# Optimization experiments

Hardware: AMD Instinct MI355X
Metric: run time of the kernel (lower is better)

## Reference

```python
import jax, jax.numpy as jnp
import numpy as np

B = 32
N_IN = 65536
N_OUT = 65536
NNZ = 2097152  # ~32 connections per output unit


def setup_inputs() -> dict:
    key = jax.random.key(0)
    k_x, k_w, k_r, k_c = jax.random.split(key, 4)
    x = jax.random.normal(k_x, (B, N_IN), dtype=jnp.float32)
    # weight init mirrors torch: randn * (init_scale / sqrt(mean_fan_in))
    init_scale = 0.01
    fan_in_mean = float(NNZ) / float(N_OUT)
    weight = jax.random.normal(k_w, (NNZ,), dtype=jnp.float32) * (init_scale / np.sqrt(fan_in_mean))
    bias = jnp.zeros((N_OUT,), dtype=jnp.float32)
    # rows are sorted (concatenated per output j in the original __init__)
    rows = jnp.sort(jax.random.randint(k_r, (NNZ,), 0, N_OUT, dtype=jnp.int64))
    cols = jax.random.randint(k_c, (NNZ,), 0, N_IN, dtype=jnp.int64)
    return {"x": x, "weight": weight, "bias": bias, "rows": rows, "cols": cols, "N_out": N_OUT}


def reference(x, weight, bias, rows, cols, N_out):
    # gather input columns per connection, scale by per-edge weight: (B, nnz)
    weighted = x[:, cols] * weight[None, :]
    # batched scatter-add by output row: segment_sum over edges -> (N_out, B) -> (B, N_out)
    out = jax.ops.segment_sum(weighted.T, rows, num_segments=N_out,
                              indices_are_sorted=True).T
    return out + bias[None, :]
```

## Files before the change

kernel.cpp:

```cpp
#include <hip/hip_runtime.h>


typedef unsigned int u32;

static __device__ __forceinline__ u32 f2bf_bits(float f) {
  u32 b = __builtin_bit_cast(u32, f);
  return (b + 0x7fffu + ((b >> 16) & 1u)) >> 16;
}
static __device__ __forceinline__ float bf_lo(u32 u) {
  return __builtin_bit_cast(float, u << 16);
}
static __device__ __forceinline__ float bf_hi(u32 u) {
  return __builtin_bit_cast(float, u & 0xffff0000u);
}

__global__ __launch_bounds__(256) void prep_kernel(
    const float* __restrict__ x, u32* __restrict__ xTb,
    const int* __restrict__ rows, int* __restrict__ row_ptr,
    int n_in, int n_out, int nnz, int tblocks) {
  if ((int)blockIdx.x < tblocks) {
    __shared__ float t[32][65];
    int c0 = blockIdx.x * 64;
    if (c0 + 64 <= n_in) {
      const float4* x4 = (const float4*)x;
      for (int idx = threadIdx.x; idx < 32 * 16; idx += 256) {
        int b = idx >> 4, q = idx & 15;
        float4 v = x4[((size_t)b * n_in + c0) / 4 + q];
        t[b][q * 4 + 0] = v.x; t[b][q * 4 + 1] = v.y;
        t[b][q * 4 + 2] = v.z; t[b][q * 4 + 3] = v.w;
      }
    } else {
      for (int idx = threadIdx.x; idx < 32 * 64; idx += 256) {
        int b = idx >> 6, cl = idx & 63;
        int c = c0 + cl;
        t[b][cl] = (c < n_in) ? x[(size_t)b * n_in + c] : 0.f;
      }
    }
    __syncthreads();
    for (int idx = threadIdx.x; idx < 64 * 16; idx += 256) {
      int cl = idx >> 4, bp = idx & 15;
      int c = c0 + cl;
      if (c < n_in) {
        u32 v = f2bf_bits(t[2 * bp][cl]) | (f2bf_bits(t[2 * bp + 1][cl]) << 16);
        xTb[(size_t)c * 16 + bp] = v;
      }
    }
  } else {
    int e = ((int)blockIdx.x - tblocks) * 256 + threadIdx.x;
    if (e < nnz) {
      int r = rows[e];
      int rp = (e == 0) ? -1 : rows[e - 1];
      for (int j = rp + 1; j <= r; ++j) row_ptr[j] = e;
      if (e == nnz - 1)
        for (int j = r + 1; j <= n_out; ++j) row_ptr[j] = nnz;
    }
  }
}

__global__ __launch_bounds__(512, 8) void ll_main_bf16_kernel(
    const uint4* __restrict__ xTb4,
    const float* __restrict__ wgt,
    const float4* __restrict__ bias4,
    const int* __restrict__ cols,
    const int* __restrict__ row_ptr,
    float4* __restrict__ out4, int n_out) {
  __shared__ float tile[32][65];
  int tid = threadIdx.x;
  int lane = tid & 63;
  int l = lane & 3;
  int gw = lane >> 2;
  int wv = tid >> 6;
  int half = wv >> 2;
  int g = (wv & 3) * 16 + gw;
  int gb = lane & 60;
  int jb = blockIdx.x * 64;
  int j = jb + g;
  float a0 = 0, a1 = 0, a2 = 0, a3 = 0, a4 = 0, a5 = 0, a6 = 0, a7 = 0;
  if (j < n_out) {
    int s = row_ptr[j], e = row_ptr[j + 1];
    int last = e - 1;
    for (int base = s + half * 4; base < e; base += 8) {
      int il = min(base + l, last);
      int cl_ = cols[il];
      float wl_ = (base + l <= last) ? wgt[il] : 0.f;
#define EDGE_K(K) { \
      int   ck = __shfl(cl_, gb | K); \
      float wk = __shfl(wl_, gb | K); \
      uint4 v  = xTb4[(size_t)ck * 4 + l]; \
      a0 = fmaf(wk, bf_lo(v.x), a0); a1 = fmaf(wk, bf_hi(v.x), a1); \
      a2 = fmaf(wk, bf_lo(v.y), a2); a3 = fmaf(wk, bf_hi(v.y), a3); \
      a4 = fmaf(wk, bf_lo(v.z), a4); a5 = fmaf(wk, bf_hi(v.z), a5); \
      a6 = fmaf(wk, bf_lo(v.w), a6); a7 = fmaf(wk, bf_hi(v.w), a7); }
      EDGE_K(0) EDGE_K(1) EDGE_K(2) EDGE_K(3)
#undef EDGE_K
    }
  }
  int b0 = l * 8;
  if (half == 0) {
    tile[b0 + 0][g] = a0; tile[b0 + 1][g] = a1; tile[b0 + 2][g] = a2; tile[b0 + 3][g] = a3;
    tile[b0 + 4][g] = a4; tile[b0 + 5][g] = a5; tile[b0 + 6][g] = a6; tile[b0 + 7][g] = a7;
  }
  __syncthreads();
  if (half == 1) {
    tile[b0 + 0][g] += a0; tile[b0 + 1][g] += a1; tile[b0 + 2][g] += a2; tile[b0 + 3][g] += a3;
    tile[b0 + 4][g] += a4; tile[b0 + 5][g] += a5; tile[b0 + 6][g] += a6; tile[b0 + 7][g] += a7;
  }
  __syncthreads();
  {
    int bb = tid >> 4, q = tid & 15;
    int jj = jb + q * 4;
    if (jj + 3 < n_out) {
      float4 bv = bias4[jj / 4];
      float4 o;
      o.x = tile[bb][q * 4 + 0] + bv.x;
      o.y = tile[bb][q * 4 + 1] + bv.y;
      o.z = tile[bb][q * 4 + 2] + bv.z;
      o.w = tile[bb][q * 4 + 3] + bv.w;
      out4[((size_t)bb * n_out + jj) / 4] = o;
    } else {
      float* out = (float*)out4;
      const float* bias = (const float*)bias4;
      for (int d = 0; d < 4; ++d)
        if (jj + d < n_out)
          out[(size_t)bb * n_out + jj + d] = tile[bb][q * 4 + d] + bias[jj + d];
    }
  }
}

__global__ __launch_bounds__(256) void transpose_x_kernel(
    const float* __restrict__ x, float* __restrict__ xT, int n_in) {
  __shared__ float t[32][65];
  int c0 = blockIdx.x * 64;
  for (int idx = threadIdx.x; idx < 32 * 64; idx += 256) {
    int b = idx >> 6, cl = idx & 63;
    int c = c0 + cl;
    t[b][cl] = (c < n_in) ? x[(size_t)b * n_in + c] : 0.0f;
  }
  __syncthreads();
  for (int idx = threadIdx.x; idx < 64 * 32; idx += 256) {
    int cl = idx >> 5, b = idx & 31;
    int c = c0 + cl;
    if (c < n_in) xT[(size_t)c * 32 + b] = t[b][cl];
  }
}

__global__ __launch_bounds__(256) void build_rowptr_bs_kernel(
    const int* __restrict__ rows, int* __restrict__ row_ptr, int nnz, int n_out) {
  int j = blockIdx.x * blockDim.x + threadIdx.x;
  if (j > n_out) return;
  int lo = 0, hi = nnz;
  while (lo < hi) { int m = (lo + hi) >> 1; if (rows[m] < j) lo = m + 1; else hi = m; }
  row_ptr[j] = lo;
}

__global__ __launch_bounds__(256) void ll_main4_kernel(
    const float4* __restrict__ xT4,
    const float* __restrict__ wgt,
    const float* __restrict__ bias,
    const int* __restrict__ cols,
    const int* __restrict__ row_ptr,
    float* __restrict__ out, int n_out) {
  __shared__ float tile[32][33];
  int tid = threadIdx.x;
  int g = tid >> 3;
  int l = tid & 7;
  int jb = blockIdx.x * 32;
  int j = jb + g;
  float ax = 0.f, ay = 0.f, az = 0.f, aw = 0.f;
  if (j < n_out) {
    int s = row_ptr[j];
    int e = row_ptr[j + 1];
    for (int base = s; base < e; base += 4) {
      int last = e - 1;
      int i1 = min(base + 1, last), i2 = min(base + 2, last), i3 = min(base + 3, last);
      int c0 = cols[base], c1 = cols[i1], c2 = cols[i2], c3 = cols[i3];
      float w0 = wgt[base];
      float w1 = (base + 1 <= last) ? wgt[i1] : 0.f;
      float w2 = (base + 2 <= last) ? wgt[i2] : 0.f;
      float w3 = (base + 3 <= last) ? wgt[i3] : 0.f;
      float4 x0 = xT4[(size_t)c0 * 8 + l];
      float4 x1 = xT4[(size_t)c1 * 8 + l];
      float4 x2 = xT4[(size_t)c2 * 8 + l];
      float4 x3 = xT4[(size_t)c3 * 8 + l];
      ax = fmaf(w0, x0.x, ax); ay = fmaf(w0, x0.y, ay);
      az = fmaf(w0, x0.z, az); aw = fmaf(w0, x0.w, aw);
      ax = fmaf(w1, x1.x, ax); ay = fmaf(w1, x1.y, ay);
      az = fmaf(w1, x1.z, az); aw = fmaf(w1, x1.w, aw);
      ax = fmaf(w2, x2.x, ax); ay = fmaf(w2, x2.y, ay);
      az = fmaf(w2, x2.z, az); aw = fmaf(w2, x2.w, aw);
      ax = fmaf(w3, x3.x, ax); ay = fmaf(w3, x3.y, ay);
      az = fmaf(w3, x3.z, az); aw = fmaf(w3, x3.w, aw);
    }
  }
  tile[l * 4 + 0][g] = ax;
  tile[l * 4 + 1][g] = ay;
  tile[l * 4 + 2][g] = az;
  tile[l * 4 + 3][g] = aw;
  __syncthreads();
  for (int idx = tid; idx < 32 * 32; idx += 256) {
    int bb = idx >> 5, jl = idx & 31;
    int jj = jb + jl;
    if (jj < n_out) out[(size_t)bb * n_out + jj] = tile[bb][jl] + bias[jj];
  }
}

__global__ __launch_bounds__(256) void ll_naive_kernel(
    const float* __restrict__ x,
    const float* __restrict__ wgt,
    const float* __restrict__ bias,
    const int* __restrict__ rows,
    const int* __restrict__ cols,
    float* __restrict__ out,
    int n_in, int n_out, int nnz, int B) {
  int idx = blockIdx.x * blockDim.x + threadIdx.x;
  if (idx >= n_out * B) return;
  int j = idx % n_out;
  int b = idx / n_out;
  int lo = 0, hi = nnz;
  while (lo < hi) { int m = (lo + hi) >> 1; if (rows[m] < j) lo = m + 1; else hi = m; }
  int s = lo;
  hi = nnz;
  while (lo < hi) { int m = (lo + hi) >> 1; if (rows[m] <= j) lo = m + 1; else hi = m; }
  int e = lo;
  float acc = 0.0f;
  for (int t = s; t < e; ++t)
    acc = fmaf(wgt[t], x[(size_t)b * n_in + cols[t]], acc);
  out[(size_t)b * n_out + j] = acc + bias[j];
}

extern "C" void kernel_launch(void* const* d_in, const int* in_sizes, int n_in_arrays,
                              void* d_out, int out_size, void* d_ws, size_t ws_size,
                              hipStream_t stream) {
  const float* x    = (const float*)d_in[0];
  const float* wgt  = (const float*)d_in[1];
  const float* bias = (const float*)d_in[2];
  const int*   rows = (const int*)d_in[3];
  const int*   cols = (const int*)d_in[4];
  float* out = (float*)d_out;

  const int nnz   = in_sizes[1];
  const int n_out = in_sizes[2];
  const int B     = out_size / n_out;
  const int n_in  = in_sizes[0] / B;

  const size_t xTb_bytes = (size_t)n_in * 32 * 2;
  const size_t xT_bytes  = (size_t)n_in * 32 * sizeof(float);
  const size_t rp_bytes  = (size_t)(n_out + 1) * sizeof(int);

  if (B == 32 && ws_size >= xTb_bytes + rp_bytes) {
    u32* xTb = (u32*)d_ws;
    int* row_ptr = (int*)((char*)d_ws + xTb_bytes);
    int tblocks = (n_in + 63) / 64;
    int eblocks = (nnz + 255) / 256;
    prep_kernel<<<tblocks + eblocks, 256, 0, stream>>>(
        x, xTb, rows, row_ptr, n_in, n_out, nnz, tblocks);
    ll_main_bf16_kernel<<<(n_out + 63) / 64, 512, 0, stream>>>(
        (const uint4*)xTb, wgt, (const float4*)bias, cols, row_ptr,
        (float4*)out, n_out);
  } else if (B == 32 && ws_size >= xT_bytes + rp_bytes) {
    float* xT = (float*)d_ws;
    int* row_ptr = (int*)((char*)d_ws + xT_bytes);
    transpose_x_kernel<<<(n_in + 63) / 64, 256, 0, stream>>>(x, xT, n_in);
    build_rowptr_bs_kernel<<<(n_out + 256) / 256, 256, 0, stream>>>(rows, row_ptr, nnz, n_out);
    ll_main4_kernel<<<(n_out + 31) / 32, 256, 0, stream>>>(
        (const float4*)xT, wgt, bias, cols, row_ptr, out, n_out);
  } else {
    int total = n_out * B;
    ll_naive_kernel<<<(total + 255) / 256, 256, 0, stream>>>(
        x, wgt, bias, rows, cols, out, n_in, n_out, nnz, B);
  }
}
```

Before: 37.84 us.

## Stage block's edge cols/weights in LDS and unroll eight gathers per iteration

Each block first copies its contiguous range of (col, weight) pairs into a shared-memory buffer with coalesced loads. The inner loop then reads edge metadata from LDS instead of shuffling per-lane global loads, and issues eight independent x gathers per iteration for more memory-level parallelism. This adds a barrier, 24KB of LDS per block that may limit occupancy, and a fallback path when a block's edge count exceeds the cap.

```diff
diff --git a/kernel.cpp b/kernel.cpp
--- a/kernel.cpp
+++ b/kernel.cpp
@@ -2,6 +2,8 @@
 
 
 typedef unsigned int u32;
+
+#define ECAP 3072
 
 static __device__ __forceinline__ u32 f2bf_bits(float f) {
   u32 b = __builtin_bit_cast(u32, f);
@@ -12,6 +14,9 @@
 }
 static __device__ __forceinline__ float bf_hi(u32 u) {
   return __builtin_bit_cast(float, u & 0xffff0000u);
+}
+static __device__ __forceinline__ float asf(u32 u) {
+  return __builtin_bit_cast(float, u);
 }
 
 __global__ __launch_bounds__(256) void prep_kernel(
@@ -57,7 +62,7 @@
   }
 }
 
-__global__ __launch_bounds__(512, 8) void ll_main_bf16_kernel(
+__global__ __launch_bounds__(512, 8) void ll_main_lds_kernel(
     const uint4* __restrict__ xTb4,
     const float* __restrict__ wgt,
     const float4* __restrict__ bias4,
@@ -65,6 +70,7 @@
     const int* __restrict__ row_ptr,
     float4* __restrict__ out4, int n_out) {
   __shared__ float tile[32][65];
+  __shared__ uint2 estage[ECAP];
   int tid = threadIdx.x;
   int lane = tid & 63;
   int l = lane & 3;
@@ -72,28 +78,68 @@
   int wv = tid >> 6;
   int half = wv >> 2;
   int g = (wv & 3) * 16 + gw;
-  int gb = lane & 60;
   int jb = blockIdx.x * 64;
+  int je = min(jb + 64, n_out);
+  int be0 = row_ptr[jb];
+  int cnt = row_ptr[je] - be0;
+  bool staged = (cnt <= ECAP);
+  if (staged) {
+    for (int t = tid; t < cnt; t += 512)
+      estage[t] = make_uint2((u32)cols[be0 + t],
+                             __builtin_bit_cast(u32, wgt[be0 + t]));
+  }
+  __syncthreads();
   int j = jb + g;
   float a0 = 0, a1 = 0, a2 = 0, a3 = 0, a4 = 0, a5 = 0, a6 = 0, a7 = 0;
   if (j < n_out) {
     int s = row_ptr[j], e = row_ptr[j + 1];
     int last = e - 1;
-    for (int base = s + half * 4; base < e; base += 8) {
-      int il = min(base + l, last);
-      int cl_ = cols[il];
-      float wl_ = (base + l <= last) ? wgt[il] : 0.f;
-#define EDGE_K(K) { \
-      int   ck = __shfl(cl_, gb | K); \
-      float wk = __shfl(wl_, gb | K); \
-      uint4 v  = xTb4[(size_t)ck * 4 + l]; \
-      a0 = fmaf(wk, bf_lo(v.x), a0); a1 = fmaf(wk, bf_hi(v.x), a1); \
-      a2 = fmaf(wk, bf_lo(v.y), a2); a3 = fmaf(wk, bf_hi(v.y), a3); \
-      a4 = fmaf(wk, bf_lo(v.z), a4); a5 = fmaf(wk, bf_hi(v.z), a5); \
-      a6 = fmaf(wk, bf_lo(v.w), a6); a7 = fmaf(wk, bf_hi(v.w), a7); }
-      EDGE_K(0) EDGE_K(1) EDGE_K(2) EDGE_K(3)
-#undef EDGE_K
-    }
+#define EDGE(V, W) \
+      a0 = fmaf(W, bf_lo(V.x), a0); a1 = fmaf(W, bf_hi(V.x), a1); \
+      a2 = fmaf(W, bf_lo(V.y), a2); a3 = fmaf(W, bf_hi(V.y), a3); \
+      a4 = fmaf(W, bf_lo(V.z), a4); a5 = fmaf(W, bf_hi(V.z), a5); \
+      a6 = fmaf(W, bf_lo(V.w), a6); a7 = fmaf(W, bf_hi(V.w), a7);
+    if (staged) {
+      const uint2* es = estage - be0;
+      for (int base = s + half * 8; base < e; base += 16) {
+        uint2 e0 = es[base];
+        uint2 e1 = es[min(base + 1, last)];
+        uint2 e2 = es[min(base + 2, last)];
+        uint2 e3 = es[min(base + 3, last)];
+        uint2 e4 = es[min(base + 4, last)];
+        uint2 e5 = es[min(base + 5, last)];
+        uint2 e6 = es[min(base + 6, last)];
+        uint2 e7 = es[min(base + 7, last)];
+        float w0 = asf(e0.y);
+        float w1 = (base + 1 <= last) ? asf(e1.y) : 0.f;
+        float w2 = (base + 2 <= last) ? asf(e2.y) : 0.f;
+        float w3 = (base + 3 <= last) ? asf(e3.y) : 0.f;
+        float w4 = (base + 4 <= last) ? asf(e4.y) : 0.f;
+        float w5 = (base + 5 <= last) ? asf(e5.y) : 0.f;
+        float w6 = (base + 6 <= last) ? asf(e6.y) : 0.f;
+        float w7 = (base + 7 <= last) ? asf(e7.y) : 0.f;
+        uint4 v0 = xTb4[(size_t)e0.x * 4 + l];
+        uint4 v1 = xTb4[(size_t)e1.x * 4 + l];
+        uint4 v2 = xTb4[(size_t)e2.x * 4 + l];
+        uint4 v3 = xTb4[(size_t)e3.x * 4 + l];
+        uint4 v4 = xTb4[(size_t)e4.x * 4 + l];
+        uint4 v5 = xTb4[(size_t)e5.x * 4 + l];
+        uint4 v6 = xTb4[(size_t)e6.x * 4 + l];
+        uint4 v7 = xTb4[(size_t)e7.x * 4 + l];
+        EDGE(v0, w0) EDGE(v1, w1) EDGE(v2, w2) EDGE(v3, w3)
+        EDGE(v4, w4) EDGE(v5, w5) EDGE(v6, w6) EDGE(v7, w7)
+      }
+    } else {
+      for (int base = s + half * 8; base < e; base += 16) {
+        for (int q = 0; q < 8; ++q) {
+          int i = min(base + q, last);
+          float w = (base + q <= last) ? wgt[i] : 0.f;
+          uint4 v = xTb4[(size_t)cols[i] * 4 + l];
+          EDGE(v, w)
+        }
+      }
+    }
+#undef EDGE
   }
   int b0 = l * 8;
   if (half == 0) {
@@ -254,7 +300,7 @@
     int eblocks = (nnz + 255) / 256;
     prep_kernel<<<tblocks + eblocks, 256, 0, stream>>>(
         x, xTb, rows, row_ptr, n_in, n_out, nnz, tblocks);
-    ll_main_bf16_kernel<<<(n_out + 63) / 64, 512, 0, stream>>>(
+    ll_main_lds_kernel<<<(n_out + 63) / 64, 512, 0, stream>>>(
         (const uint4*)xTb, wgt, (const float4*)bias, cols, row_ptr,
         (float4*)out, n_out);
   } else if (B == 32 && ws_size >= xT_bytes + rp_bytes) {
```

Result: slower. 73.63 us (+94.6%).

## Split batch into two 16-column passes over half-size transposed bf16 input

Applied to the files above, without the earlier changes.

The bf16 transposed input is stored as two separate halves of 16 batch columns each, and the main SpMM kernel now runs twice, once per half, each pass accumulating four outputs per thread. The intent is to shrink the gathered working set per pass (2 MB instead of 4 MB) so random column gathers hit cache more often. In exchange, cols, weights and row_ptr are read twice, an extra kernel launch is added, and the launch-bounds occupancy hint is dropped.

```diff
diff --git a/kernel.cpp b/kernel.cpp
--- a/kernel.cpp
+++ b/kernel.cpp
@@ -15,7 +15,7 @@
 }
 
 __global__ __launch_bounds__(256) void prep_kernel(
-    const float* __restrict__ x, u32* __restrict__ xTb,
+    const float* __restrict__ x, u32* __restrict__ xTb0, u32* __restrict__ xTb1,
     const int* __restrict__ rows, int* __restrict__ row_ptr,
     int n_in, int n_out, int nnz, int tblocks) {
   if ((int)blockIdx.x < tblocks) {
@@ -42,7 +42,8 @@
       int c = c0 + cl;
       if (c < n_in) {
         u32 v = f2bf_bits(t[2 * bp][cl]) | (f2bf_bits(t[2 * bp + 1][cl]) << 16);
-        xTb[(size_t)c * 16 + bp] = v;
+        u32* dst = (bp < 8) ? xTb0 : xTb1;
+        dst[(size_t)c * 8 + (bp & 7)] = v;
       }
     }
   } else {
@@ -57,14 +58,14 @@
   }
 }
 
-__global__ __launch_bounds__(512, 8) void ll_main_bf16_kernel(
-    const uint4* __restrict__ xTb4,
+__global__ __launch_bounds__(512) void ll_pass_kernel(
+    const uint2* __restrict__ xTp2,
     const float* __restrict__ wgt,
     const float4* __restrict__ bias4,
     const int* __restrict__ cols,
     const int* __restrict__ row_ptr,
-    float4* __restrict__ out4, int n_out) {
-  __shared__ float tile[32][65];
+    float4* __restrict__ out4, int n_out, int pass) {
+  __shared__ float tile[16][65];
   int tid = threadIdx.x;
   int lane = tid & 63;
   int l = lane & 3;
@@ -75,7 +76,7 @@
   int gb = lane & 60;
   int jb = blockIdx.x * 64;
   int j = jb + g;
-  float a0 = 0, a1 = 0, a2 = 0, a3 = 0, a4 = 0, a5 = 0, a6 = 0, a7 = 0;
+  float a0 = 0, a1 = 0, a2 = 0, a3 = 0;
   if (j < n_out) {
     int s = row_ptr[j], e = row_ptr[j + 1];
     int last = e - 1;
@@ -86,29 +87,28 @@
 #define EDGE_K(K) { \
       int   ck = __shfl(cl_, gb | K); \
       float wk = __shfl(wl_, gb | K); \
-      uint4 v  = xTb4[(size_t)ck * 4 + l]; \
+      uint2 v  = xTp2[(size_t)ck * 4 + l]; \
       a0 = fmaf(wk, bf_lo(v.x), a0); a1 = fmaf(wk, bf_hi(v.x), a1); \
-      a2 = fmaf(wk, bf_lo(v.y), a2); a3 = fmaf(wk, bf_hi(v.y), a3); \
-      a4 = fmaf(wk, bf_lo(v.z), a4); a5 = fmaf(wk, bf_hi(v.z), a5); \
-      a6 = fmaf(wk, bf_lo(v.w), a6); a7 = fmaf(wk, bf_hi(v.w), a7); }
+      a2 = fmaf(wk, bf_lo(v.y), a2); a3 = fmaf(wk, bf_hi(v.y), a3); }
       EDGE_K(0) EDGE_K(1) EDGE_K(2) EDGE_K(3)
 #undef EDGE_K
     }
   }
-  int b0 = l * 8;
+  int b0 = l * 4;
   if (half == 0) {
-    tile[b0 + 0][g] = a0; tile[b0 + 1][g] = a1; tile[b0 + 2][g] = a2; tile[b0 + 3][g] = a3;
-    tile[b0 + 4][g] = a4; tile[b0 + 5][g] = a5; tile[b0 + 6][g] = a6; tile[b0 + 7][g] = a7;
+    tile[b0 + 0][g] = a0; tile[b0 + 1][g] = a1;
+    tile[b0 + 2][g] = a2; tile[b0 + 3][g] = a3;
   }
   __syncthreads();
   if (half == 1) {
-    tile[b0 + 0][g] += a0; tile[b0 + 1][g] += a1; tile[b0 + 2][g] += a2; tile[b0 + 3][g] += a3;
-    tile[b0 + 4][g] += a4; tile[b0 + 5][g] += a5; tile[b0 + 6][g] += a6; tile[b0 + 7][g] += a7;
-  }
-  __syncthreads();
-  {
+    tile[b0 + 0][g] += a0; tile[b0 + 1][g] += a1;
+    tile[b0 + 2][g] += a2; tile[b0 + 3][g] += a3;
+  }
+  __syncthreads();
+  if (tid < 256) {
     int bb = tid >> 4, q = tid & 15;
     int jj = jb + q * 4;
+    int brow = pass * 16 + bb;
     if (jj + 3 < n_out) {
       float4 bv = bias4[jj / 4];
       float4 o;
@@ -116,13 +116,13 @@
       o.y = tile[bb][q * 4 + 1] + bv.y;
       o.z = tile[bb][q * 4 + 2] + bv.z;
       o.w = tile[bb][q * 4 + 3] + bv.w;
-      out4[((size_t)bb * n_out + jj) / 4] = o;
+      out4[((size_t)brow * n_out + jj) / 4] = o;
     } else {
       float* out = (float*)out4;
       const float* bias = (const float*)bias4;
       for (int d = 0; d < 4; ++d)
         if (jj + d < n_out)
-          out[(size_t)bb * n_out + jj + d] = tile[bb][q * 4 + d] + bias[jj + d];
+          out[(size_t)brow * n_out + jj + d] = tile[bb][q * 4 + d] + bias[jj + d];
     }
   }
 }
@@ -243,20 +243,25 @@
   const int B     = out_size / n_out;
   const int n_in  = in_sizes[0] / B;
 
-  const size_t xTb_bytes = (size_t)n_in * 32 * 2;
-  const size_t xT_bytes  = (size_t)n_in * 32 * sizeof(float);
-  const size_t rp_bytes  = (size_t)(n_out + 1) * sizeof(int);
-
-  if (B == 32 && ws_size >= xTb_bytes + rp_bytes) {
-    u32* xTb = (u32*)d_ws;
-    int* row_ptr = (int*)((char*)d_ws + xTb_bytes);
+  const size_t half_bytes = (size_t)n_in * 8 * sizeof(u32);
+  const size_t xT_bytes   = (size_t)n_in * 32 * sizeof(float);
+  const size_t rp_bytes   = (size_t)(n_out + 1) * sizeof(int);
+
+  if (B == 32 && ws_size >= 2 * half_bytes + rp_bytes) {
+    u32* xTb0 = (u32*)d_ws;
+    u32* xTb1 = (u32*)((char*)d_ws + half_bytes);
+    int* row_ptr = (int*)((char*)d_ws + 2 * half_bytes);
     int tblocks = (n_in + 63) / 64;
     int eblocks = (nnz + 255) / 256;
     prep_kernel<<<tblocks + eblocks, 256, 0, stream>>>(
-        x, xTb, rows, row_ptr, n_in, n_out, nnz, tblocks);
-    ll_main_bf16_kernel<<<(n_out + 63) / 64, 512, 0, stream>>>(
-        (const uint4*)xTb, wgt, (const float4*)bias, cols, row_ptr,
-        (float4*)out, n_out);
+        x, xTb0, xTb1, rows, row_ptr, n_in, n_out, nnz, tblocks);
+    int jblocks = (n_out + 63) / 64;
+    ll_pass_kernel<<<jblocks, 512, 0, stream>>>(
+        (const uint2*)xTb0, wgt, (const float4*)bias, cols, row_ptr,
+        (float4*)out, n_out, 0);
+    ll_pass_kernel<<<jblocks, 512, 0, stream>>>(
+        (const uint2*)xTb1, wgt, (const float4*)bias, cols, row_ptr,
+        (float4*)out, n_out, 1);
   } else if (B == 32 && ws_size >= xT_bytes + rp_bytes) {
     float* xT = (float*)d_ws;
     int* row_ptr = (int*)((char*)d_ws + xT_bytes);
```

New measurement: 48.48 us. 1.28x slower.
